# Kernel optimization log

Measured on AMD Instinct MI355X. Metric: run time of the kernel, lower is better.

Reference implementation:

```python
import jax, jax.numpy as jnp
import numpy as np

EPS = 1e-5  # BatchNorm eps

def _gcn_norm(edge_index, edge_weight, n):
    # PyG gcn_norm with add_self_loops=True, fill_value=1.0
    loop = jnp.arange(n, dtype=edge_index.dtype)
    row = jnp.concatenate([edge_index[0], loop])
    col = jnp.concatenate([edge_index[1], loop])
    ew = jnp.concatenate([edge_weight, jnp.ones((n,), edge_weight.dtype)])
    deg = jax.ops.segment_sum(ew, col, num_segments=n)
    dis = jnp.where(deg > 0, jax.lax.rsqrt(jnp.maximum(deg, 1e-30)), 0.0)
    norm = dis[row] * ew * dis[col]
    return row, col, norm

def _gcn_conv(x, W, b, row, col, norm, n):
    h = x @ W                               # [N, out]
    msg = h[row] * norm[:, None]            # gather + edge scale
    out = jax.ops.segment_sum(msg, col, num_segments=n)
    return out + b

def _bn_eval(x, gamma, beta, mean, var):
    return (x - mean) * jax.lax.rsqrt(var + EPS) * gamma + beta

def setup_inputs() -> dict:
    key = jax.random.key(0)
    ks = jax.random.split(key, 12)
    N, E, V, H = 100000, 1600000, 256, 128
    x = jax.random.normal(ks[0], (N, V), jnp.float32)
    edge_index = jax.random.randint(ks[1], (2, E), 0, N, jnp.int64)
    edge_weight = jax.random.uniform(ks[2], (E,), jnp.float32)
    s = lambda fan: 1.0 / np.sqrt(fan)
    return {
        "x": x, "edge_index": edge_index, "edge_weight": edge_weight,
        "W1": jax.random.normal(ks[3], (V, H), jnp.float32) * s(V),
        "b1": jnp.zeros((H,), jnp.float32),
        "W2": jax.random.normal(ks[4], (H, H), jnp.float32) * s(H),
        "b2": jnp.zeros((H,), jnp.float32),
        "W3": jax.random.normal(ks[5], (H, 1), jnp.float32) * s(H),
        "b3": jnp.zeros((1,), jnp.float32),
        "Wres": jax.random.normal(ks[6], (V, H), jnp.float32) * s(V),
        "g1": jnp.ones((H,), jnp.float32), "be1": jnp.zeros((H,), jnp.float32),
        "m1": jax.random.normal(ks[7], (H,), jnp.float32) * 0.01,
        "v1": jnp.ones((H,), jnp.float32),
        "g2": jnp.ones((H,), jnp.float32), "be2": jnp.zeros((H,), jnp.float32),
        "m2": jax.random.normal(ks[8], (H,), jnp.float32) * 0.01,
        "v2": jnp.ones((H,), jnp.float32),
    }

def reference(x, edge_index, edge_weight, W1, b1, W2, b2, W3, b3, Wres,
              g1, be1, m1, v1, g2, be2, m2, v2):
    n = x.shape[0]
    row, col, norm = _gcn_norm(edge_index, edge_weight, n)
    res = x @ Wres                                   # residual branch
    h = _gcn_conv(x, W1, b1, row, col, norm, n)
    h = jax.nn.relu(_bn_eval(h, g1, be1, m1, v1))    # dropout off (eval)
    h = _gcn_conv(h, W2, b2, row, col, norm, n) + res
    h = jax.nn.relu(_bn_eval(h, g2, be2, m2, v2))
    h = _gcn_conv(h, W3, b3, row, col, norm, n)      # [N, 1]
    return jnp.squeeze(h, axis=1)
```

## Files before the change

### kernel.cpp

```cpp
#include <hip/hip_runtime.h>
#include <hip/hip_bf16.h>

#define BN_EPS 1e-5f

using short8 = __attribute__((ext_vector_type(8))) short;
using f32x4  = __attribute__((ext_vector_type(4))) float;

#define FIX_SCALE 262144.0f
#define FIX_MASK  0x01ffffffu
#define CNT_ONE   (1u << 25)

static __device__ __forceinline__ unsigned short f2bf(float f) {
  unsigned int u = __float_as_uint(f);
  unsigned int r = (u + 0x7fffu + ((u >> 16) & 1u)) >> 16;
  return (unsigned short)r;
}


static __global__ void cast_weights(const float* __restrict__ W1, const float* __restrict__ Wres,
                                    const float* __restrict__ W2,
                                    unsigned short* __restrict__ BT1,
                                    unsigned short* __restrict__ BT2) {
  int i = blockIdx.x * blockDim.x + threadIdx.x;
  if (i < 256 * 256) {
    int n = i >> 8, k = i & 255;
    float v = (n < 128) ? W1[k * 128 + n] : Wres[k * 128 + (n - 128)];
    BT1[i] = f2bf(v);
  } else if (i < 256 * 256 + 128 * 128) {
    int j = i - 256 * 256;
    int n = j >> 7, k = j & 127;
    BT2[j] = f2bf(W2[k * 128 + n]);
  }
}


static __global__ __launch_bounds__(256)
void fused_gemm1_hist(const float* __restrict__ A, const unsigned short* __restrict__ BT,
                      unsigned short* __restrict__ C0, unsigned short* __restrict__ C1, int M,
                      const int* __restrict__ col, const float* __restrict__ ew,
                      unsigned int* __restrict__ packed,
                      unsigned short* __restrict__ rank, int E, int gB) {
  __shared__ unsigned short As[64 * 40];
  __shared__ unsigned short Bs[256 * 40];

  int b = blockIdx.x;
  if (b >= gB) {
    int e = (b - gB) * blockDim.x + threadIdx.x;
    if (e < E) {
      int c = col[e];
      unsigned int fx = (unsigned int)(ew[e] * FIX_SCALE + 0.5f);
      unsigned int old = atomicAdd(&packed[c], CNT_ONE | fx);
      rank[e] = (unsigned short)(old >> 25);
    }
    return;
  }

  int t = threadIdx.x;
  int wv = t >> 6, lane = t & 63;
  int quad = lane >> 4, l15 = lane & 15;
  int m0 = b * 64;

  f32x4 acc[4][4];
#pragma unroll
  for (int i = 0; i < 4; ++i)
#pragma unroll
    for (int j = 0; j < 4; ++j) acc[i][j] = (f32x4){0.f, 0.f, 0.f, 0.f};

  int ar = t >> 2;
  int ac = (t & 3) * 8;
  bool avalid = (m0 + ar) < M;
  const float* Arow = A + (size_t)(m0 + ar) * 256 + ac;
  const unsigned short* Brow = BT + (size_t)t * 256;

  float4 a0 = make_float4(0.f, 0.f, 0.f, 0.f), a1 = a0;
  if (avalid) {
    a0 = *(const float4*)(Arow + 0);
    a1 = *(const float4*)(Arow + 4);
  }
  short8 b0 = *(const short8*)(Brow + 0);
  short8 b1 = *(const short8*)(Brow + 8);
  short8 b2 = *(const short8*)(Brow + 16);
  short8 b3 = *(const short8*)(Brow + 24);

  for (int k0 = 0; k0 < 256; k0 += 32) {
    short8 av;
    av[0] = (short)f2bf(a0.x); av[1] = (short)f2bf(a0.y);
    av[2] = (short)f2bf(a0.z); av[3] = (short)f2bf(a0.w);
    av[4] = (short)f2bf(a1.x); av[5] = (short)f2bf(a1.y);
    av[6] = (short)f2bf(a1.z); av[7] = (short)f2bf(a1.w);
    *(short8*)&As[ar * 40 + ac] = av;
    *(short8*)&Bs[t * 40 + 0]  = b0;
    *(short8*)&Bs[t * 40 + 8]  = b1;
    *(short8*)&Bs[t * 40 + 16] = b2;
    *(short8*)&Bs[t * 40 + 24] = b3;
    __syncthreads();

    if (k0 + 32 < 256) {
      int kn = k0 + 32;
      if (avalid) {
        a0 = *(const float4*)(Arow + kn);
        a1 = *(const float4*)(Arow + kn + 4);
      }
      b0 = *(const short8*)(Brow + kn);
      b1 = *(const short8*)(Brow + kn + 8);
      b2 = *(const short8*)(Brow + kn + 16);
      b3 = *(const short8*)(Brow + kn + 24);
    }

    short8 af[4], bf[4];
#pragma unroll
    for (int mt = 0; mt < 4; ++mt)
      af[mt] = *(const short8*)&As[(mt * 16 + l15) * 40 + quad * 8];
#pragma unroll
    for (int nt = 0; nt < 4; ++nt)
      bf[nt] = *(const short8*)&Bs[(wv * 64 + nt * 16 + l15) * 40 + quad * 8];
#pragma unroll
    for (int mt = 0; mt < 4; ++mt)
#pragma unroll
      for (int nt = 0; nt < 4; ++nt)
        acc[mt][nt] = __builtin_amdgcn_mfma_f32_16x16x32_bf16(af[mt], bf[nt], acc[mt][nt], 0, 0, 0);
    __syncthreads();
  }

  int nbase = wv * 64;
#pragma unroll
  for (int mt = 0; mt < 4; ++mt) {
#pragma unroll
    for (int nt = 0; nt < 4; ++nt) {
      int n = nbase + nt * 16 + l15;
#pragma unroll
      for (int reg = 0; reg < 4; ++reg) {
        size_t m = (size_t)(m0 + mt * 16 + quad * 4 + reg);
        if (nbase < 128) C0[m * 128 + n] = f2bf(acc[mt][nt][reg]);
        else             C1[m * 128 + (n - 128)] = f2bf(acc[mt][nt][reg]);
      }
    }
  }
}


#define SCAN_B 256
#define SCAN_I 4
static __global__ void scanA(const unsigned int* __restrict__ packed,
                             float* __restrict__ dis, int* __restrict__ cnt,
                             int* __restrict__ start, int* __restrict__ blkSum, int N) {
  __shared__ int sh[SCAN_B];
  int t = threadIdx.x;
  int base = blockIdx.x * SCAN_B * SCAN_I + t * SCAN_I;
  int v[SCAN_I];
  int tot = 0;
#pragma unroll
  for (int j = 0; j < SCAN_I; ++j) {
    if (base + j < N) {
      unsigned int pv = packed[base + j];
      v[j] = (int)(pv >> 25);
      cnt[base + j] = v[j];
      float deg = 1.0f + (float)(pv & FIX_MASK) * (1.0f / FIX_SCALE);
      dis[base + j] = rsqrtf(deg);
    } else v[j] = 0;
    tot += v[j];
  }
  sh[t] = tot;
  __syncthreads();
  int self = tot;
  for (int off = 1; off < SCAN_B; off <<= 1) {
    int add = (t >= off) ? sh[t - off] : 0;
    __syncthreads();
    sh[t] += add;
    __syncthreads();
  }
  int excl = sh[t] - self;
  if (t == SCAN_B - 1) blkSum[blockIdx.x] = sh[t];
  int run = excl;
#pragma unroll
  for (int j = 0; j < SCAN_I; ++j) {
    if (base + j < N) start[base + j] = run;
    run += v[j];
  }
}

static __global__ void scanB(const int* __restrict__ blkSum, int* __restrict__ blkOff, int nb) {
  __shared__ int sh[256];
  int t = threadIdx.x;
  int v = (t < nb) ? blkSum[t] : 0;
  sh[t] = v;
  __syncthreads();
  for (int off = 1; off < 256; off <<= 1) {
    int add = (t >= off) ? sh[t - off] : 0;
    __syncthreads();
    sh[t] += add;
    __syncthreads();
  }
  if (t < nb) blkOff[t] = sh[t] - v;
}

static __global__ void scanC(int* start, const int* __restrict__ blkOff, int N) {
  int i = blockIdx.x * blockDim.x + threadIdx.x;
  if (i < N) start[i] += blkOff[i / (SCAN_B * SCAN_I)];
}

static __global__ void place_kernel(const int* __restrict__ row, const int* __restrict__ col,
                                    const float* __restrict__ ew, const float* __restrict__ dis,
                                    const int* __restrict__ start,
                                    const unsigned short* __restrict__ rank,
                                    long long* __restrict__ edges, int E) {
  int e = blockIdx.x * blockDim.x + threadIdx.x;
  if (e < E) {
    int r = row[e], c = col[e];
    int pos = start[c] + (int)rank[e];
    float nrm = dis[r] * ew[e];
    long long v = ((long long)__float_as_int(nrm) << 32) | (unsigned int)r;
    __builtin_nontemporal_store(v, &edges[pos]);
  }
}


static __global__ __launch_bounds__(256)
void gemm2_mfma(const unsigned short* __restrict__ A, const unsigned short* __restrict__ BT,
                unsigned short* __restrict__ C) {
  __shared__ unsigned short As[128 * 40];
  __shared__ unsigned short Bs[128 * 40];
  int t = threadIdx.x;
  int wv = t >> 6, lane = t & 63;
  int quad = lane >> 4, l15 = lane & 15;
  int m0 = blockIdx.x * 128;

  f32x4 acc[4][4];
#pragma unroll
  for (int i = 0; i < 4; ++i)
#pragma unroll
    for (int j = 0; j < 4; ++j) acc[i][j] = (f32x4){0.f, 0.f, 0.f, 0.f};

  int sr = t >> 1, sc = (t & 1) * 16;

  for (int k0 = 0; k0 < 128; k0 += 32) {
    short8 a0 = *(const short8*)(A + (size_t)(m0 + sr) * 128 + k0 + sc);
    short8 a1 = *(const short8*)(A + (size_t)(m0 + sr) * 128 + k0 + sc + 8);
    *(short8*)&As[sr * 40 + sc]     = a0;
    *(short8*)&As[sr * 40 + sc + 8] = a1;
    short8 b0 = *(const short8*)(BT + (size_t)sr * 128 + k0 + sc);
    short8 b1 = *(const short8*)(BT + (size_t)sr * 128 + k0 + sc + 8);
    *(short8*)&Bs[sr * 40 + sc]     = b0;
    *(short8*)&Bs[sr * 40 + sc + 8] = b1;
    __syncthreads();

    int mb = (wv >> 1) * 64, nb = (wv & 1) * 64;
    short8 af[4], bf[4];
#pragma unroll
    for (int mt = 0; mt < 4; ++mt)
      af[mt] = *(const short8*)&As[(mb + mt * 16 + l15) * 40 + quad * 8];
#pragma unroll
    for (int nt = 0; nt < 4; ++nt)
      bf[nt] = *(const short8*)&Bs[(nb + nt * 16 + l15) * 40 + quad * 8];
#pragma unroll
    for (int mt = 0; mt < 4; ++mt)
#pragma unroll
      for (int nt = 0; nt < 4; ++nt)
        acc[mt][nt] = __builtin_amdgcn_mfma_f32_16x16x32_bf16(af[mt], bf[nt], acc[mt][nt], 0, 0, 0);
    __syncthreads();
  }

  int mb = (wv >> 1) * 64, nb = (wv & 1) * 64;
#pragma unroll
  for (int mt = 0; mt < 4; ++mt)
#pragma unroll
    for (int nt = 0; nt < 4; ++nt) {
      int n = nb + nt * 16 + l15;
#pragma unroll
      for (int reg = 0; reg < 4; ++reg) {
        size_t m = (size_t)(m0 + mb + mt * 16 + quad * 4 + reg);
        C[m * 128 + n] = f2bf(acc[mt][nt][reg]);
      }
    }
}


#define PROP_GATHER_BODY                                                        \
  int c0 = lane * 2;                                                            \
  float d = dis[w];                                                             \
  float acc0, acc1;                                                             \
  {                                                                             \
    unsigned int u = Hsrc[(size_t)w * 64 + lane];                               \
    acc0 = d * __uint_as_float(u << 16);                                        \
    acc1 = d * __uint_as_float(u & 0xffff0000u);                                \
  }                                                                             \
  int s = start[w], n = cnt[w];                                                 \
  int k = 0;                                                                    \
  while (k < n) {                                                               \
    int chunk = min(n - k, 64);                                                 \
    int idx = 0;                                                                \
    float wt = 0.f;                                                             \
    if (lane < chunk) {                                                         \
      long long ev = edges[s + k + lane];                                       \
      idx = (int)(unsigned int)(ev & 0xffffffffLL);                             \
      wt  = __int_as_float((int)(ev >> 32));                                    \
    }                                                                           \
    for (int j = 0; j < chunk; j += 8) {                                        \
      int   i0 = __shfl(idx, j + 0, 64), i1 = __shfl(idx, j + 1, 64);           \
      int   i2 = __shfl(idx, j + 2, 64), i3 = __shfl(idx, j + 3, 64);           \
      int   i4 = __shfl(idx, j + 4, 64), i5 = __shfl(idx, j + 5, 64);           \
      int   i6 = __shfl(idx, j + 6, 64), i7 = __shfl(idx, j + 7, 64);           \
      float w0 = __shfl(wt, j + 0, 64), w1 = __shfl(wt, j + 1, 64);             \
      float w2 = __shfl(wt, j + 2, 64), w3 = __shfl(wt, j + 3, 64);             \
      float w4 = __shfl(wt, j + 4, 64), w5 = __shfl(wt, j + 5, 64);             \
      float w6 = __shfl(wt, j + 6, 64), w7 = __shfl(wt, j + 7, 64);             \
      unsigned int u0 = Hsrc[(size_t)i0 * 64 + lane];                           \
      unsigned int u1 = Hsrc[(size_t)i1 * 64 + lane];                           \
      unsigned int u2 = Hsrc[(size_t)i2 * 64 + lane];                           \
      unsigned int u3 = Hsrc[(size_t)i3 * 64 + lane];                           \
      unsigned int u4 = Hsrc[(size_t)i4 * 64 + lane];                           \
      unsigned int u5 = Hsrc[(size_t)i5 * 64 + lane];                           \
      unsigned int u6 = Hsrc[(size_t)i6 * 64 + lane];                           \
      unsigned int u7 = Hsrc[(size_t)i7 * 64 + lane];                           \
      acc0 = fmaf(w0, __uint_as_float(u0 << 16), acc0);                         \
      acc1 = fmaf(w0, __uint_as_float(u0 & 0xffff0000u), acc1);                 \
      acc0 = fmaf(w1, __uint_as_float(u1 << 16), acc0);                         \
      acc1 = fmaf(w1, __uint_as_float(u1 & 0xffff0000u), acc1);                 \
      acc0 = fmaf(w2, __uint_as_float(u2 << 16), acc0);                         \
      acc1 = fmaf(w2, __uint_as_float(u2 & 0xffff0000u), acc1);                 \
      acc0 = fmaf(w3, __uint_as_float(u3 << 16), acc0);                         \
      acc1 = fmaf(w3, __uint_as_float(u3 & 0xffff0000u), acc1);                 \
      acc0 = fmaf(w4, __uint_as_float(u4 << 16), acc0);                         \
      acc1 = fmaf(w4, __uint_as_float(u4 & 0xffff0000u), acc1);                 \
      acc0 = fmaf(w5, __uint_as_float(u5 << 16), acc0);                         \
      acc1 = fmaf(w5, __uint_as_float(u5 & 0xffff0000u), acc1);                 \
      acc0 = fmaf(w6, __uint_as_float(u6 << 16), acc0);                         \
      acc1 = fmaf(w6, __uint_as_float(u6 & 0xffff0000u), acc1);                 \
      acc0 = fmaf(w7, __uint_as_float(u7 << 16), acc0);                         \
      acc1 = fmaf(w7, __uint_as_float(u7 & 0xffff0000u), acc1);                 \
    }                                                                           \
    k += chunk;                                                                 \
  }                                                                             \
  acc0 *= d;                                                                    \
  acc1 *= d;

static __global__ __launch_bounds__(256)
void prop128_bf16out(const unsigned int* __restrict__ Hsrc,
                     const int* __restrict__ start, const int* __restrict__ cnt,
                     const long long* __restrict__ edges,
                     const float* __restrict__ dis,
                     const float* __restrict__ bvec,
                     const float* __restrict__ g, const float* __restrict__ be,
                     const float* __restrict__ mean, const float* __restrict__ var,
                     unsigned int* __restrict__ Outb, int N) {
  int w = (int)((blockIdx.x * blockDim.x + threadIdx.x) >> 6);
  int lane = threadIdx.x & 63;
  if (w >= N) return;
  PROP_GATHER_BODY
  float x0 = acc0 + bvec[c0];
  float x1 = acc1 + bvec[c0 + 1];
  float s0 = g[c0] * rsqrtf(var[c0] + BN_EPS);
  float s1 = g[c0 + 1] * rsqrtf(var[c0 + 1] + BN_EPS);
  x0 = fmaxf((x0 - mean[c0]) * s0 + be[c0], 0.f);
  x1 = fmaxf((x1 - mean[c0 + 1]) * s1 + be[c0 + 1], 0.f);
  unsigned int packed = (unsigned int)f2bf(x0) | ((unsigned int)f2bf(x1) << 16);
  Outb[(size_t)w * 64 + lane] = packed;
}

static __global__ __launch_bounds__(256)
void prop128_w3out(const unsigned int* __restrict__ Hsrc,
                   const int* __restrict__ start, const int* __restrict__ cnt,
                   const long long* __restrict__ edges,
                   const float* __restrict__ dis,
                   const float* __restrict__ bvec,
                   const float* __restrict__ g, const float* __restrict__ be,
                   const float* __restrict__ mean, const float* __restrict__ var,
                   const unsigned int* __restrict__ resb, const float* __restrict__ W3,
                   float* __restrict__ h3, int N) {
  int w = (int)((blockIdx.x * blockDim.x + threadIdx.x) >> 6);
  int lane = threadIdx.x & 63;
  if (w >= N) return;
  PROP_GATHER_BODY
  unsigned int ru = resb[(size_t)w * 64 + lane];
  float x0 = acc0 + bvec[c0]     + __uint_as_float(ru << 16);
  float x1 = acc1 + bvec[c0 + 1] + __uint_as_float(ru & 0xffff0000u);
  float s0 = g[c0] * rsqrtf(var[c0] + BN_EPS);
  float s1 = g[c0 + 1] * rsqrtf(var[c0 + 1] + BN_EPS);
  x0 = fmaxf((x0 - mean[c0]) * s0 + be[c0], 0.f);
  x1 = fmaxf((x1 - mean[c0 + 1]) * s1 + be[c0 + 1], 0.f);
  float v = x0 * W3[c0] + x1 * W3[c0 + 1];
#pragma unroll
  for (int off = 32; off > 0; off >>= 1) v += __shfl_down(v, off, 64);
  if (lane == 0) h3[w] = v;
}


static __global__ void prop3_kernel(const float* __restrict__ h3,
                                    const int* __restrict__ start, const int* __restrict__ cnt,
                                    const long long* __restrict__ edges,
                                    const float* __restrict__ dis, const float* __restrict__ b3,
                                    float* __restrict__ out, int N) {
  int i = blockIdx.x * blockDim.x + threadIdx.x;
  if (i >= N) return;
  float d = dis[i];
  float acc = d * h3[i];
  int s = start[i], n = cnt[i];
  for (int k = 0; k < n; ++k) {
    long long ev = edges[s + k];
    int src = (int)(unsigned int)(ev & 0xffffffffLL);
    float wt = __int_as_float((int)(ev >> 32));
    acc = fmaf(wt, h3[src], acc);
  }
  out[i] = acc * d + b3[0];
}


extern "C" void kernel_launch(void* const* d_in, const int* in_sizes, int n_in,
                              void* d_out, int out_size, void* d_ws, size_t ws_size,
                              hipStream_t stream) {
  const float* x    = (const float*)d_in[0];
  const int*   ei   = (const int*)d_in[1];
  const float* ew   = (const float*)d_in[2];
  const float* W1   = (const float*)d_in[3];
  const float* b1   = (const float*)d_in[4];
  const float* W2   = (const float*)d_in[5];
  const float* b2   = (const float*)d_in[6];
  const float* W3   = (const float*)d_in[7];
  const float* b3   = (const float*)d_in[8];
  const float* Wres = (const float*)d_in[9];
  const float* g1   = (const float*)d_in[10];
  const float* be1  = (const float*)d_in[11];
  const float* m1   = (const float*)d_in[12];
  const float* v1   = (const float*)d_in[13];
  const float* g2   = (const float*)d_in[14];
  const float* be2  = (const float*)d_in[15];
  const float* m2   = (const float*)d_in[16];
  const float* v2   = (const float*)d_in[17];

  int Hh = in_sizes[4];
  int V  = in_sizes[3] / Hh;
  int N  = in_sizes[0] / V;
  int E  = in_sizes[2];
  const int* row = ei;
  const int* col = ei + E;

  int Mp = ((N + 127) / 128) * 128;

  char* p = (char*)d_ws;
  auto alloc = [&](size_t bytes) -> char* {
    char* r = p;
    p += (bytes + 255) & ~(size_t)255;
    return r;
  };
  unsigned int* packed = (unsigned int*)alloc((size_t)N * 4);
  float* dis    = (float*)alloc((size_t)N * 4);
  int*   cnt    = (int*)  alloc((size_t)N * 4);
  int*   startA = (int*)  alloc((size_t)N * 4);
  int*   blkSum = (int*)  alloc(256 * 4);
  int*   blkOff = (int*)  alloc(256 * 4);
  unsigned short* rank = (unsigned short*)alloc((size_t)E * 2);
  long long* edges = (long long*)alloc((size_t)E * 8);
  float* h3     = (float*)alloc((size_t)N * 4);
  unsigned short* BT1 = (unsigned short*)alloc((size_t)256 * 256 * 2);
  unsigned short* BT2 = (unsigned short*)alloc((size_t)128 * 128 * 2);
  unsigned short* bufG  = (unsigned short*)alloc((size_t)Mp * 128 * 2);
  unsigned short* bufH1 = (unsigned short*)alloc((size_t)Mp * 128 * 2);
  unsigned short* bufRes = (unsigned short*)alloc((size_t)Mp * 128 * 2);
  (void)ws_size; (void)n_in; (void)out_size;

  int TB = 256;
  hipMemsetAsync(packed, 0, (size_t)N * 4, stream);
  cast_weights<<<(256 * 256 + 128 * 128 + TB - 1) / TB, TB, 0, stream>>>(W1, Wres, W2, BT1, BT2);

  int gB = Mp / 64;
  int hB = (E + TB - 1) / TB;
  fused_gemm1_hist<<<gB + hB, TB, 0, stream>>>(x, BT1, bufG, bufRes, N,
                                               col, ew, packed, rank, E, gB);

  int nb = (N + SCAN_B * SCAN_I - 1) / (SCAN_B * SCAN_I);
  scanA<<<nb, SCAN_B, 0, stream>>>(packed, dis, cnt, startA, blkSum, N);
  scanB<<<1, 256, 0, stream>>>(blkSum, blkOff, nb);
  scanC<<<(N + TB - 1) / TB, TB, 0, stream>>>(startA, blkOff, N);
  place_kernel<<<(E + TB - 1) / TB, TB, 0, stream>>>(row, col, ew, dis, startA,
                                                     rank, edges, E);

  int propBlocks = (int)(((size_t)N * 64 + TB - 1) / TB);
  prop128_bf16out<<<propBlocks, TB, 0, stream>>>((const unsigned int*)bufG, startA, cnt,
                                                 edges, dis, b1, g1, be1, m1, v1,
                                                 (unsigned int*)bufH1, N);

  gemm2_mfma<<<Mp / 128, 256, 0, stream>>>(bufH1, BT2, bufG);

  prop128_w3out<<<propBlocks, TB, 0, stream>>>((const unsigned int*)bufG, startA, cnt,
                                               edges, dis, b2, g2, be2, m2, v2,
                                               (const unsigned int*)bufRes, W3, h3, N);

  prop3_kernel<<<(N + TB - 1) / TB, TB, 0, stream>>>(h3, startA, cnt, edges,
                                                     dis, b3, (float*)d_out, N);
}
```

Measured before the change: 491.1 us.

## Split degree histogram into four sub-counters and stream pre-laid-out weights in GEMM1

The degree/rank histogram now spreads atomics over four copies per node (picked by edge index mod 4), which cuts same-address atomic contention. The scan runs over the 4N sub-counters, so each (node, copy) pair gets its own start offset while each node's edges stay contiguous. GEMM1 now reads weight fragments straight from global memory in a k-blocked layout instead of staging B in shared memory, and double-buffers the A tile with one sync per step. In exchange, the histogram and scan touch four times as much memory, and the B reads lose shared-memory reuse across the block.

```diff
diff --git a/kernel.cpp b/kernel.cpp
--- a/kernel.cpp
+++ b/kernel.cpp
@@ -19,13 +19,13 @@
 
 static __global__ void cast_weights(const float* __restrict__ W1, const float* __restrict__ Wres,
                                     const float* __restrict__ W2,
-                                    unsigned short* __restrict__ BT1,
+                                    unsigned short* __restrict__ B2,
                                     unsigned short* __restrict__ BT2) {
   int i = blockIdx.x * blockDim.x + threadIdx.x;
   if (i < 256 * 256) {
     int n = i >> 8, k = i & 255;
     float v = (n < 128) ? W1[k * 128 + n] : Wres[k * 128 + (n - 128)];
-    BT1[i] = f2bf(v);
+    B2[(k >> 5) * 8192 + n * 32 + (k & 31)] = f2bf(v);
   } else if (i < 256 * 256 + 128 * 128) {
     int j = i - 256 * 256;
     int n = j >> 7, k = j & 127;
@@ -35,22 +35,25 @@
 
 
 static __global__ __launch_bounds__(256)
-void fused_gemm1_hist(const float* __restrict__ A, const unsigned short* __restrict__ BT,
+void fused_gemm1_hist(const float* __restrict__ A, const unsigned short* __restrict__ B2,
                       unsigned short* __restrict__ C0, unsigned short* __restrict__ C1, int M,
                       const int* __restrict__ col, const float* __restrict__ ew,
                       unsigned int* __restrict__ packed,
-                      unsigned short* __restrict__ rank, int E, int gB) {
-  __shared__ unsigned short As[64 * 40];
-  __shared__ unsigned short Bs[256 * 40];
+                      unsigned short* __restrict__ rank, int E, int gB, int N) {
+  __shared__ unsigned short As[2 * 64 * 40];
 
   int b = blockIdx.x;
   if (b >= gB) {
-    int e = (b - gB) * blockDim.x + threadIdx.x;
-    if (e < E) {
-      int c = col[e];
-      unsigned int fx = (unsigned int)(ew[e] * FIX_SCALE + 0.5f);
-      unsigned int old = atomicAdd(&packed[c], CNT_ONE | fx);
-      rank[e] = (unsigned short)(old >> 25);
+    int base = (b - gB) * (256 * 4) + threadIdx.x;
+#pragma unroll
+    for (int j = 0; j < 4; ++j) {
+      int e = base + j * 256;
+      if (e < E) {
+        int c = col[e];
+        unsigned int fx = (unsigned int)(ew[e] * FIX_SCALE + 0.5f);
+        unsigned int old = atomicAdd(&packed[(size_t)(e & 3) * N + c], CNT_ONE | fx);
+        rank[e] = (unsigned short)(old >> 25);
+      }
     }
     return;
   }
@@ -70,55 +73,55 @@
   int ac = (t & 3) * 8;
   bool avalid = (m0 + ar) < M;
   const float* Arow = A + (size_t)(m0 + ar) * 256 + ac;
-  const unsigned short* Brow = BT + (size_t)t * 256;
+  const unsigned short* Bfrag = B2 + (wv * 64 + l15) * 32 + quad * 8;
 
   float4 a0 = make_float4(0.f, 0.f, 0.f, 0.f), a1 = a0;
   if (avalid) {
     a0 = *(const float4*)(Arow + 0);
     a1 = *(const float4*)(Arow + 4);
   }
-  short8 b0 = *(const short8*)(Brow + 0);
-  short8 b1 = *(const short8*)(Brow + 8);
-  short8 b2 = *(const short8*)(Brow + 16);
-  short8 b3 = *(const short8*)(Brow + 24);
-
-  for (int k0 = 0; k0 < 256; k0 += 32) {
+  {
     short8 av;
     av[0] = (short)f2bf(a0.x); av[1] = (short)f2bf(a0.y);
     av[2] = (short)f2bf(a0.z); av[3] = (short)f2bf(a0.w);
     av[4] = (short)f2bf(a1.x); av[5] = (short)f2bf(a1.y);
     av[6] = (short)f2bf(a1.z); av[7] = (short)f2bf(a1.w);
     *(short8*)&As[ar * 40 + ac] = av;
-    *(short8*)&Bs[t * 40 + 0]  = b0;
-    *(short8*)&Bs[t * 40 + 8]  = b1;
-    *(short8*)&Bs[t * 40 + 16] = b2;
-    *(short8*)&Bs[t * 40 + 24] = b3;
-    __syncthreads();
-
-    if (k0 + 32 < 256) {
-      int kn = k0 + 32;
-      if (avalid) {
-        a0 = *(const float4*)(Arow + kn);
-        a1 = *(const float4*)(Arow + kn + 4);
-      }
-      b0 = *(const short8*)(Brow + kn);
-      b1 = *(const short8*)(Brow + kn + 8);
-      b2 = *(const short8*)(Brow + kn + 16);
-      b3 = *(const short8*)(Brow + kn + 24);
+  }
+  __syncthreads();
+
+#pragma unroll 2
+  for (int s = 0; s < 8; ++s) {
+    int cur = (s & 1) ? 2560 : 0;
+
+    short8 bf[4];
+#pragma unroll
+    for (int nt = 0; nt < 4; ++nt)
+      bf[nt] = *(const short8*)(Bfrag + s * 8192 + nt * 512);
+
+    if (s < 7 && avalid) {
+      a0 = *(const float4*)(Arow + (s + 1) * 32);
+      a1 = *(const float4*)(Arow + (s + 1) * 32 + 4);
     }
 
-    short8 af[4], bf[4];
+    short8 af[4];
 #pragma unroll
     for (int mt = 0; mt < 4; ++mt)
-      af[mt] = *(const short8*)&As[(mt * 16 + l15) * 40 + quad * 8];
-#pragma unroll
-    for (int nt = 0; nt < 4; ++nt)
-      bf[nt] = *(const short8*)&Bs[(wv * 64 + nt * 16 + l15) * 40 + quad * 8];
+      af[mt] = *(const short8*)&As[cur + (mt * 16 + l15) * 40 + quad * 8];
 #pragma unroll
     for (int mt = 0; mt < 4; ++mt)
 #pragma unroll
       for (int nt = 0; nt < 4; ++nt)
         acc[mt][nt] = __builtin_amdgcn_mfma_f32_16x16x32_bf16(af[mt], bf[nt], acc[mt][nt], 0, 0, 0);
+
+    if (s < 7) {
+      short8 av;
+      av[0] = (short)f2bf(a0.x); av[1] = (short)f2bf(a0.y);
+      av[2] = (short)f2bf(a0.z); av[3] = (short)f2bf(a0.w);
+      av[4] = (short)f2bf(a1.x); av[5] = (short)f2bf(a1.y);
+      av[6] = (short)f2bf(a1.z); av[7] = (short)f2bf(a1.w);
+      *(short8*)&As[(cur ^ 2560) + ar * 40 + ac] = av;
+    }
     __syncthreads();
   }
 
@@ -140,25 +143,36 @@
 
 
 #define SCAN_B 256
-#define SCAN_I 4
+#define SCAN_I 8
 static __global__ void scanA(const unsigned int* __restrict__ packed,
                              float* __restrict__ dis, int* __restrict__ cnt,
-                             int* __restrict__ start, int* __restrict__ blkSum, int N) {
+                             int* __restrict__ startV, int* __restrict__ blkSum, int N) {
   __shared__ int sh[SCAN_B];
   int t = threadIdx.x;
-  int base = blockIdx.x * SCAN_B * SCAN_I + t * SCAN_I;
+  int vbase = blockIdx.x * (SCAN_B * SCAN_I) + t * SCAN_I;
   int v[SCAN_I];
   int tot = 0;
 #pragma unroll
-  for (int j = 0; j < SCAN_I; ++j) {
-    if (base + j < N) {
-      unsigned int pv = packed[base + j];
-      v[j] = (int)(pv >> 25);
-      cnt[base + j] = v[j];
-      float deg = 1.0f + (float)(pv & FIX_MASK) * (1.0f / FIX_SCALE);
-      dis[base + j] = rsqrtf(deg);
-    } else v[j] = 0;
-    tot += v[j];
+  for (int g = 0; g < SCAN_I / 4; ++g) {
+    int c = (vbase >> 2) + g;
+    int csum = 0;
+    if (c < N) {
+      unsigned int usum = 0;
+#pragma unroll
+      for (int r = 0; r < 4; ++r) {
+        unsigned int pv = packed[(size_t)r * N + c];
+        int cr = (int)(pv >> 25);
+        v[g * 4 + r] = cr;
+        csum += cr;
+        usum += (pv & FIX_MASK);
+      }
+      cnt[c] = csum;
+      dis[c] = rsqrtf(1.0f + (float)usum * (1.0f / FIX_SCALE));
+    } else {
+#pragma unroll
+      for (int r = 0; r < 4; ++r) v[g * 4 + r] = 0;
+    }
+    tot += csum;
   }
   sh[t] = tot;
   __syncthreads();
@@ -174,7 +188,7 @@
   int run = excl;
 #pragma unroll
   for (int j = 0; j < SCAN_I; ++j) {
-    if (base + j < N) start[base + j] = run;
+    if (vbase + j < 4 * N) startV[vbase + j] = run;
     run += v[j];
   }
 }
@@ -194,20 +208,20 @@
   if (t < nb) blkOff[t] = sh[t] - v;
 }
 
-static __global__ void scanC(int* start, const int* __restrict__ blkOff, int N) {
+static __global__ void scanC(int* startV, const int* __restrict__ blkOff, int NV) {
   int i = blockIdx.x * blockDim.x + threadIdx.x;
-  if (i < N) start[i] += blkOff[i / (SCAN_B * SCAN_I)];
+  if (i < NV) startV[i] += blkOff[i / (SCAN_B * SCAN_I)];
 }
 
 static __global__ void place_kernel(const int* __restrict__ row, const int* __restrict__ col,
                                     const float* __restrict__ ew, const float* __restrict__ dis,
-                                    const int* __restrict__ start,
+                                    const int* __restrict__ startV,
                                     const unsigned short* __restrict__ rank,
                                     long long* __restrict__ edges, int E) {
   int e = blockIdx.x * blockDim.x + threadIdx.x;
   if (e < E) {
     int r = row[e], c = col[e];
-    int pos = start[c] + (int)rank[e];
+    int pos = startV[c * 4 + (e & 3)] + (int)rank[e];
     float nrm = dis[r] * ew[e];
     long long v = ((long long)__float_as_int(nrm) << 32) | (unsigned int)r;
     __builtin_nontemporal_store(v, &edges[pos]);
@@ -284,7 +298,7 @@
     acc0 = d * __uint_as_float(u << 16);                                        \
     acc1 = d * __uint_as_float(u & 0xffff0000u);                                \
   }                                                                             \
-  int s = start[w], n = cnt[w];                                                 \
+  int s = start4[(size_t)w * 4], n = cnt[w];                                    \
   int k = 0;                                                                    \
   while (k < n) {                                                               \
     int chunk = min(n - k, 64);                                                 \
@@ -336,7 +350,7 @@
 
 static __global__ __launch_bounds__(256)
 void prop128_bf16out(const unsigned int* __restrict__ Hsrc,
-                     const int* __restrict__ start, const int* __restrict__ cnt,
+                     const int* __restrict__ start4, const int* __restrict__ cnt,
                      const long long* __restrict__ edges,
                      const float* __restrict__ dis,
                      const float* __restrict__ bvec,
@@ -359,7 +373,7 @@
 
 static __global__ __launch_bounds__(256)
 void prop128_w3out(const unsigned int* __restrict__ Hsrc,
-                   const int* __restrict__ start, const int* __restrict__ cnt,
+                   const int* __restrict__ start4, const int* __restrict__ cnt,
                    const long long* __restrict__ edges,
                    const float* __restrict__ dis,
                    const float* __restrict__ bvec,
@@ -386,7 +400,7 @@
 
 
 static __global__ void prop3_kernel(const float* __restrict__ h3,
-                                    const int* __restrict__ start, const int* __restrict__ cnt,
+                                    const int* __restrict__ start4, const int* __restrict__ cnt,
                                     const long long* __restrict__ edges,
                                     const float* __restrict__ dis, const float* __restrict__ b3,
                                     float* __restrict__ out, int N) {
@@ -394,7 +408,7 @@
   if (i >= N) return;
   float d = dis[i];
   float acc = d * h3[i];
-  int s = start[i], n = cnt[i];
+  int s = start4[(size_t)i * 4], n = cnt[i];
   for (int k = 0; k < n; ++k) {
     long long ev = edges[s + k];
     int src = (int)(unsigned int)(ev & 0xffffffffLL);
@@ -442,16 +456,16 @@
     p += (bytes + 255) & ~(size_t)255;
     return r;
   };
-  unsigned int* packed = (unsigned int*)alloc((size_t)N * 4);
+  unsigned int* packed = (unsigned int*)alloc((size_t)N * 4 * 4);
   float* dis    = (float*)alloc((size_t)N * 4);
   int*   cnt    = (int*)  alloc((size_t)N * 4);
-  int*   startA = (int*)  alloc((size_t)N * 4);
+  int*   startV = (int*)  alloc((size_t)N * 4 * 4);
   int*   blkSum = (int*)  alloc(256 * 4);
   int*   blkOff = (int*)  alloc(256 * 4);
   unsigned short* rank = (unsigned short*)alloc((size_t)E * 2);
   long long* edges = (long long*)alloc((size_t)E * 8);
   float* h3     = (float*)alloc((size_t)N * 4);
-  unsigned short* BT1 = (unsigned short*)alloc((size_t)256 * 256 * 2);
+  unsigned short* B2  = (unsigned short*)alloc((size_t)256 * 256 * 2);
   unsigned short* BT2 = (unsigned short*)alloc((size_t)128 * 128 * 2);
   unsigned short* bufG  = (unsigned short*)alloc((size_t)Mp * 128 * 2);
   unsigned short* bufH1 = (unsigned short*)alloc((size_t)Mp * 128 * 2);
@@ -459,32 +473,33 @@
   (void)ws_size; (void)n_in; (void)out_size;
 
   int TB = 256;
-  hipMemsetAsync(packed, 0, (size_t)N * 4, stream);
-  cast_weights<<<(256 * 256 + 128 * 128 + TB - 1) / TB, TB, 0, stream>>>(W1, Wres, W2, BT1, BT2);
+  hipMemsetAsync(packed, 0, (size_t)N * 4 * 4, stream);
+  cast_weights<<<(256 * 256 + 128 * 128 + TB - 1) / TB, TB, 0, stream>>>(W1, Wres, W2, B2, BT2);
 
   int gB = Mp / 64;
-  int hB = (E + TB - 1) / TB;
-  fused_gemm1_hist<<<gB + hB, TB, 0, stream>>>(x, BT1, bufG, bufRes, N,
-                                               col, ew, packed, rank, E, gB);
-
-  int nb = (N + SCAN_B * SCAN_I - 1) / (SCAN_B * SCAN_I);
-  scanA<<<nb, SCAN_B, 0, stream>>>(packed, dis, cnt, startA, blkSum, N);
+  int hB = (E + TB * 4 - 1) / (TB * 4);
+  fused_gemm1_hist<<<gB + hB, TB, 0, stream>>>(x, B2, bufG, bufRes, N,
+                                               col, ew, packed, rank, E, gB, N);
+
+  int NV = 4 * N;
+  int nb = (NV + SCAN_B * SCAN_I - 1) / (SCAN_B * SCAN_I);
+  scanA<<<nb, SCAN_B, 0, stream>>>(packed, dis, cnt, startV, blkSum, N);
   scanB<<<1, 256, 0, stream>>>(blkSum, blkOff, nb);
-  scanC<<<(N + TB - 1) / TB, TB, 0, stream>>>(startA, blkOff, N);
-  place_kernel<<<(E + TB - 1) / TB, TB, 0, stream>>>(row, col, ew, dis, startA,
+  scanC<<<(NV + TB - 1) / TB, TB, 0, stream>>>(startV, blkOff, NV);
+  place_kernel<<<(E + TB - 1) / TB, TB, 0, stream>>>(row, col, ew, dis, startV,
                                                      rank, edges, E);
 
   int propBlocks = (int)(((size_t)N * 64 + TB - 1) / TB);
-  prop128_bf16out<<<propBlocks, TB, 0, stream>>>((const unsigned int*)bufG, startA, cnt,
+  prop128_bf16out<<<propBlocks, TB, 0, stream>>>((const unsigned int*)bufG, startV, cnt,
                                                  edges, dis, b1, g1, be1, m1, v1,
                                                  (unsigned int*)bufH1, N);
 
   gemm2_mfma<<<Mp / 128, 256, 0, stream>>>(bufH1, BT2, bufG);
 
-  prop128_w3out<<<propBlocks, TB, 0, stream>>>((const unsigned int*)bufG, startA, cnt,
+  prop128_w3out<<<propBlocks, TB, 0, stream>>>((const unsigned int*)bufG, startV, cnt,
                                                edges, dis, b2, g2, be2, m2, v2,
                                                (const unsigned int*)bufRes, W3, h3, N);
 
-  prop3_kernel<<<(N + TB - 1) / TB, TB, 0, stream>>>(h3, startA, cnt, edges,
+  prop3_kernel<<<(N + TB - 1) / TB, TB, 0, stream>>>(h3, startV, cnt, edges,
                                                      dis, b3, (float*)d_out, N);
 }
```

Measured after the change: 489.5 us. About the same (-0.3%).
